# Kernel optimization log

Measured on AMD Instinct MI355X. Metric: run time of the kernel, lower is better.

The kernel has to match this reference:

```python
import jax, jax.numpy as jnp
import numpy as np

IN_F = 4096
OUT_F = 4096
BATCH = 1024

def setup_inputs() -> dict:
    key = jax.random.key(0)
    k = jax.random.split(key, 7)
    x = jax.random.normal(k[0], (BATCH, IN_F), dtype=jnp.float32)
    weight_mu = jax.random.normal(k[1], (OUT_F, IN_F), dtype=jnp.float32) * (1.0 / np.sqrt(IN_F))
    # torch init: uniform(-5,-3) for sigma params (raw values, used directly as std)
    weight_sigma = jax.random.uniform(k[2], (OUT_F, IN_F), dtype=jnp.float32, minval=-5.0, maxval=-3.0)
    bias_mu = jnp.zeros((OUT_F,), dtype=jnp.float32)
    bias_sigma = jax.random.uniform(k[3], (OUT_F,), dtype=jnp.float32, minval=-5.0, maxval=-3.0)
    eps_w = jax.random.normal(k[4], (OUT_F, IN_F), dtype=jnp.float32)
    eps_b = jax.random.normal(k[5], (OUT_F,), dtype=jnp.float32)
    return {"x": x, "weight_mu": weight_mu, "weight_sigma": weight_sigma,
            "bias_mu": bias_mu, "bias_sigma": bias_sigma,
            "eps_w": eps_w, "eps_b": eps_b}

def reference(x, weight_mu, weight_sigma, bias_mu, bias_sigma, eps_w, eps_b):
    # training-mode forward: reparameterized weight sample then dense matmul
    weight = weight_mu + eps_w * weight_sigma        # [out, in]
    bias = bias_mu + eps_b * bias_sigma              # [out]
    # F.linear(x, W, b) = x @ W.T + b
    return jnp.einsum('bi,oi->bo', x, weight) + bias
```

## Files before the change

kernel.cpp:

```cpp
#include <hip/hip_runtime.h>
#include <hip/hip_bf16.h>
#include <stdint.h>

#define M_BATCH 1024
#define N_OUT   4096
#define K_IN    4096

#define BM 128
#define BN 128
#define BK 64
#define KPER  (K_IN / 2)
#define KITER (KPER / BK)

typedef __attribute__((ext_vector_type(8))) __bf16 bf16x8_t;
typedef __attribute__((ext_vector_type(4))) float f32x4_t;
typedef __attribute__((ext_vector_type(4))) float fvec4;

__device__ __forceinline__ unsigned short f2bf_bits(float f) {
    union { __hip_bfloat16 h; unsigned short u; } cvt;
    cvt.h = __float2bfloat16(f);
    return cvt.u;
}

struct __align__(8) US4 { unsigned short x, y, z, w; };

__global__ __launch_bounds__(256) void prep_kernel(
    const float* __restrict__ x,
    const float* __restrict__ wmu,
    const float* __restrict__ wsig,
    const float* __restrict__ epsw,
    unsigned short* __restrict__ wb,
    unsigned short* __restrict__ xb)
{
    const size_t tid = (size_t)blockIdx.x * blockDim.x + threadIdx.x;
    const size_t T   = (size_t)1048576;

    const fvec4* wmu4  = (const fvec4*)wmu;
    const fvec4* wsig4 = (const fvec4*)wsig;
    const fvec4* epsw4 = (const fvec4*)epsw;
    US4* wb4 = (US4*)wb;

    fvec4 m[4], s[4], e[4];
    #pragma unroll
    for (int r = 0; r < 4; ++r) {
        const size_t i = tid + (size_t)r * T;
        m[r] = __builtin_nontemporal_load(wmu4  + i);
        s[r] = __builtin_nontemporal_load(wsig4 + i);
        e[r] = __builtin_nontemporal_load(epsw4 + i);
    }
    #pragma unroll
    for (int r = 0; r < 4; ++r) {
        US4 o;
        o.x = f2bf_bits(fmaf(e[r].x, s[r].x, m[r].x));
        o.y = f2bf_bits(fmaf(e[r].y, s[r].y, m[r].y));
        o.z = f2bf_bits(fmaf(e[r].z, s[r].z, m[r].z));
        o.w = f2bf_bits(fmaf(e[r].w, s[r].w, m[r].w));
        wb4[tid + (size_t)r * T] = o;
    }

    fvec4 v = __builtin_nontemporal_load((const fvec4*)x + tid);
    US4 o;
    o.x = f2bf_bits(v.x);
    o.y = f2bf_bits(v.y);
    o.z = f2bf_bits(v.z);
    o.w = f2bf_bits(v.w);
    ((US4*)xb)[tid] = o;
}

__global__ __launch_bounds__(512, 2) void gemm_bt_kernel(
    const unsigned short* __restrict__ A,
    const unsigned short* __restrict__ B,
    const float* __restrict__ bmu,
    const float* __restrict__ bsig,
    const float* __restrict__ ebias,
    float* __restrict__ C)
{
    __shared__ unsigned short lds[2 * 32768];

    const int t     = threadIdx.x;
    const int bm0   = blockIdx.y * BM;
    const int bn0   = blockIdx.x * BN;
    const int lane  = t & 63;
    const int wave  = t >> 6;
    const int khalf = wave >> 2;
    const int quadw = wave & 3;
    const int wrow  = (quadw >> 1) * 64;
    const int wcol  = (quadw & 1) * 64;
    const int lm    = lane & 15;
    const int quad  = lane >> 4;

    f32x4_t acc[4][4] = {};

    const unsigned short* srcs[8];
    const int rlow = t >> 3;
    const int jsw  = ((t & 7) ^ (rlow & 7)) * 8;
    #pragma unroll
    for (int s = 0; s < 8; ++s) {
        const int row  = rlow + (s & 1) * 64;
        const int half = (s >> 1) & 1;
        const unsigned short* base = (s < 4)
            ? (A + (size_t)(bm0 + row) * K_IN)
            : (B + (size_t)(bn0 + row) * K_IN);
        srcs[s] = base + half * KPER + jsw;
    }
    char* dst0 = (char*)lds + t * 16;

    #pragma unroll
    for (int s = 0; s < 8; ++s)
        __builtin_amdgcn_global_load_lds(
            (const __attribute__((address_space(1))) void*)(srcs[s]),
            (__attribute__((address_space(3))) void*)(dst0 + s * 8192), 16, 0, 0);

    for (int it = 0; it < KITER; ++it) {
        __syncthreads();

        if (it + 1 < KITER) {
            const int koff = (it + 1) * BK;
            const int nb   = ((it + 1) & 1) * 65536;
            #pragma unroll
            for (int s = 0; s < 8; ++s)
                __builtin_amdgcn_global_load_lds(
                    (const __attribute__((address_space(1))) void*)(srcs[s] + koff),
                    (__attribute__((address_space(3))) void*)(dst0 + nb + s * 8192), 16, 0, 0);
        }

        const unsigned short* Lb = lds + (it & 1) * 32768;
        const unsigned short* Ah = Lb + khalf * 8192;
        const unsigned short* Bh = Lb + 16384 + khalf * 8192;

        #pragma unroll
        for (int kk = 0; kk < 2; ++kk) {
            const int p = ((kk * 4) + quad) ^ (lm & 7);
            bf16x8_t a_frag[4], b_frag[4];
            #pragma unroll
            for (int im = 0; im < 4; im++)
                a_frag[im] = *(const bf16x8_t*)(Ah + ((wrow + im * 16 + lm) * 8 + p) * 8);
            #pragma unroll
            for (int jn = 0; jn < 4; jn++)
                b_frag[jn] = *(const bf16x8_t*)(Bh + ((wcol + jn * 16 + lm) * 8 + p) * 8);
            #pragma unroll
            for (int im = 0; im < 4; im++)
                #pragma unroll
                for (int jn = 0; jn < 4; jn++)
                    acc[im][jn] = __builtin_amdgcn_mfma_f32_16x16x32_bf16(
                        a_frag[im], b_frag[jn], acc[im][jn], 0, 0, 0);
        }
    }

    f32x4_t* red = (f32x4_t*)lds;
    if (wave >= 4) {
        #pragma unroll
        for (int im = 0; im < 4; im++)
            #pragma unroll
            for (int jn = 0; jn < 4; jn++)
                red[quadw * 1024 + (im * 4 + jn) * 64 + lane] = acc[im][jn];
    }
    __syncthreads();
    if (wave < 4) {
        #pragma unroll
        for (int jn = 0; jn < 4; jn++) {
            const int gn = bn0 + wcol + jn * 16 + lm;
            const float bias = bmu[gn] + ebias[gn] * bsig[gn];
            #pragma unroll
            for (int im = 0; im < 4; im++) {
                const f32x4_t part = red[quadw * 1024 + (im * 4 + jn) * 64 + lane];
                const int gm0 = bm0 + wrow + im * 16 + quad * 4;
                #pragma unroll
                for (int r = 0; r < 4; r++)
                    C[(size_t)(gm0 + r) * N_OUT + gn] = acc[im][jn][r] + part[r] + bias;
            }
        }
    }
}

__global__ __launch_bounds__(256) void naive_kernel(
    const float* __restrict__ x, const float* __restrict__ wmu,
    const float* __restrict__ wsig, const float* __restrict__ bmu,
    const float* __restrict__ bsig, const float* __restrict__ epsw,
    const float* __restrict__ epsb, float* __restrict__ out)
{
    const int o = blockIdx.x * blockDim.x + threadIdx.x;
    const int b = blockIdx.y;
    const float4* xr = (const float4*)(x + (size_t)b * K_IN);
    const float4* mr = (const float4*)(wmu + (size_t)o * K_IN);
    const float4* sr = (const float4*)(wsig + (size_t)o * K_IN);
    const float4* er = (const float4*)(epsw + (size_t)o * K_IN);
    float s = 0.f;
    for (int k = 0; k < K_IN / 4; k++) {
        float4 xv = xr[k], m = mr[k], sg = sr[k], e = er[k];
        s += xv.x * fmaf(e.x, sg.x, m.x);
        s += xv.y * fmaf(e.y, sg.y, m.y);
        s += xv.z * fmaf(e.z, sg.z, m.z);
        s += xv.w * fmaf(e.w, sg.w, m.w);
    }
    out[(size_t)b * N_OUT + o] = s + bmu[o] + epsb[o] * bsig[o];
}

extern "C" void kernel_launch(void* const* d_in, const int* in_sizes, int n_in,
                              void* d_out, int out_size, void* d_ws, size_t ws_size,
                              hipStream_t stream)
{
    const float* x    = (const float*)d_in[0];
    const float* wmu  = (const float*)d_in[1];
    const float* wsig = (const float*)d_in[2];
    const float* bmu  = (const float*)d_in[3];
    const float* bsig = (const float*)d_in[4];
    const float* epsw = (const float*)d_in[5];
    const float* epsb = (const float*)d_in[6];
    float* out = (float*)d_out;

    const size_t need = ((size_t)N_OUT * K_IN + (size_t)M_BATCH * K_IN) * sizeof(unsigned short);
    if (ws_size >= need) {
        unsigned short* wb = (unsigned short*)d_ws;
        unsigned short* xb = wb + (size_t)N_OUT * K_IN;
        prep_kernel<<<4096, 256, 0, stream>>>(x, wmu, wsig, epsw, wb, xb);
        dim3 grid(N_OUT / BN, M_BATCH / BM);
        gemm_bt_kernel<<<grid, 512, 0, stream>>>(xb, wb, bmu, bsig, epsb, out);
    } else {
        dim3 grid(N_OUT / 256, M_BATCH);
        naive_kernel<<<grid, 256, 0, stream>>>(x, wmu, wsig, bmu, bsig, epsw, epsb, out);
    }
}
```

Before: 242.7 us.

## Fuse prep and GEMM into one cooperative kernel with grid sync

Result: slower. 301.4 us (+24.2%).

```diff
diff --git a/kernel.cpp b/kernel.cpp
--- a/kernel.cpp
+++ b/kernel.cpp
@@ -1,6 +1,9 @@
 #include <hip/hip_runtime.h>
 #include <hip/hip_bf16.h>
+#include <hip/hip_cooperative_groups.h>
 #include <stdint.h>
+
+namespace cg = cooperative_groups;
 
 #define M_BATCH 1024
 #define N_OUT   4096
@@ -22,64 +25,84 @@
     return cvt.u;
 }
 
-struct __align__(8) US4 { unsigned short x, y, z, w; };
-
-__global__ __launch_bounds__(256) void prep_kernel(
+struct __align__(16) US8 { unsigned short s[8]; };
+
+__global__ __launch_bounds__(512, 2) void fused_kernel(
     const float* __restrict__ x,
     const float* __restrict__ wmu,
     const float* __restrict__ wsig,
-    const float* __restrict__ epsw,
-    unsigned short* __restrict__ wb,
-    unsigned short* __restrict__ xb)
-{
-    const size_t tid = (size_t)blockIdx.x * blockDim.x + threadIdx.x;
-    const size_t T   = (size_t)1048576;
-
-    const fvec4* wmu4  = (const fvec4*)wmu;
-    const fvec4* wsig4 = (const fvec4*)wsig;
-    const fvec4* epsw4 = (const fvec4*)epsw;
-    US4* wb4 = (US4*)wb;
-
-    fvec4 m[4], s[4], e[4];
-    #pragma unroll
-    for (int r = 0; r < 4; ++r) {
-        const size_t i = tid + (size_t)r * T;
-        m[r] = __builtin_nontemporal_load(wmu4  + i);
-        s[r] = __builtin_nontemporal_load(wsig4 + i);
-        e[r] = __builtin_nontemporal_load(epsw4 + i);
-    }
-    #pragma unroll
-    for (int r = 0; r < 4; ++r) {
-        US4 o;
-        o.x = f2bf_bits(fmaf(e[r].x, s[r].x, m[r].x));
-        o.y = f2bf_bits(fmaf(e[r].y, s[r].y, m[r].y));
-        o.z = f2bf_bits(fmaf(e[r].z, s[r].z, m[r].z));
-        o.w = f2bf_bits(fmaf(e[r].w, s[r].w, m[r].w));
-        wb4[tid + (size_t)r * T] = o;
-    }
-
-    fvec4 v = __builtin_nontemporal_load((const fvec4*)x + tid);
-    US4 o;
-    o.x = f2bf_bits(v.x);
-    o.y = f2bf_bits(v.y);
-    o.z = f2bf_bits(v.z);
-    o.w = f2bf_bits(v.w);
-    ((US4*)xb)[tid] = o;
-}
-
-__global__ __launch_bounds__(512, 2) void gemm_bt_kernel(
-    const unsigned short* __restrict__ A,
-    const unsigned short* __restrict__ B,
     const float* __restrict__ bmu,
     const float* __restrict__ bsig,
-    const float* __restrict__ ebias,
+    const float* __restrict__ epsw,
+    const float* __restrict__ epsb,
+    unsigned short* __restrict__ wb,
+    unsigned short* __restrict__ xb,
     float* __restrict__ C)
 {
     __shared__ unsigned short lds[2 * 32768];
 
-    const int t     = threadIdx.x;
-    const int bm0   = blockIdx.y * BM;
-    const int bn0   = blockIdx.x * BN;
+    const int t  = threadIdx.x;
+    const int bx = blockIdx.x;
+    const int bn = bx & 31;
+    const int bm = bx >> 5;
+
+    {
+        const size_t base4 = (size_t)bn * 131072 + (size_t)bm * 16384;
+        const size_t base8 = (size_t)bn * 65536  + (size_t)bm * 8192;
+        const fvec4* mu4 = (const fvec4*)wmu;
+        const fvec4* sg4 = (const fvec4*)wsig;
+        const fvec4* ep4 = (const fvec4*)epsw;
+        US8* wb8 = (US8*)wb;
+        #pragma unroll
+        for (int c = 0; c < 16; ++c) {
+            const int u = c * 512 + t;
+            const size_t i4 = base4 + (size_t)u * 2;
+            fvec4 m0 = __builtin_nontemporal_load(mu4 + i4);
+            fvec4 m1 = __builtin_nontemporal_load(mu4 + i4 + 1);
+            fvec4 s0 = __builtin_nontemporal_load(sg4 + i4);
+            fvec4 s1 = __builtin_nontemporal_load(sg4 + i4 + 1);
+            fvec4 e0 = __builtin_nontemporal_load(ep4 + i4);
+            fvec4 e1 = __builtin_nontemporal_load(ep4 + i4 + 1);
+            US8 o;
+            o.s[0] = f2bf_bits(fmaf(e0.x, s0.x, m0.x));
+            o.s[1] = f2bf_bits(fmaf(e0.y, s0.y, m0.y));
+            o.s[2] = f2bf_bits(fmaf(e0.z, s0.z, m0.z));
+            o.s[3] = f2bf_bits(fmaf(e0.w, s0.w, m0.w));
+            o.s[4] = f2bf_bits(fmaf(e1.x, s1.x, m1.x));
+            o.s[5] = f2bf_bits(fmaf(e1.y, s1.y, m1.y));
+            o.s[6] = f2bf_bits(fmaf(e1.z, s1.z, m1.z));
+            o.s[7] = f2bf_bits(fmaf(e1.w, s1.w, m1.w));
+            wb8[base8 + u] = o;
+        }
+
+        const size_t xbase8 = (size_t)bm * 65536 + (size_t)bn * 2048;
+        const fvec4* x4 = (const fvec4*)x;
+        US8* xb8 = (US8*)xb;
+        #pragma unroll
+        for (int c = 0; c < 4; ++c) {
+            const int u = c * 512 + t;
+            const size_t i4 = (xbase8 + u) * 2;
+            fvec4 v0 = __builtin_nontemporal_load(x4 + i4);
+            fvec4 v1 = __builtin_nontemporal_load(x4 + i4 + 1);
+            US8 o;
+            o.s[0] = f2bf_bits(v0.x);
+            o.s[1] = f2bf_bits(v0.y);
+            o.s[2] = f2bf_bits(v0.z);
+            o.s[3] = f2bf_bits(v0.w);
+            o.s[4] = f2bf_bits(v1.x);
+            o.s[5] = f2bf_bits(v1.y);
+            o.s[6] = f2bf_bits(v1.z);
+            o.s[7] = f2bf_bits(v1.w);
+            xb8[xbase8 + u] = o;
+        }
+    }
+
+    cg::this_grid().sync();
+
+    const unsigned short* A = xb;
+    const unsigned short* B = wb;
+    const int bm0   = bm * BM;
+    const int bn0   = bn * BN;
     const int lane  = t & 63;
     const int wave  = t >> 6;
     const int khalf = wave >> 2;
@@ -160,7 +183,7 @@
         #pragma unroll
         for (int jn = 0; jn < 4; jn++) {
             const int gn = bn0 + wcol + jn * 16 + lm;
-            const float bias = bmu[gn] + ebias[gn] * bsig[gn];
+            const float bias = bmu[gn] + epsb[gn] * bsig[gn];
             #pragma unroll
             for (int im = 0; im < 4; im++) {
                 const f32x4_t part = red[quadw * 1024 + (im * 4 + jn) * 64 + lane];
@@ -213,9 +236,11 @@
     if (ws_size >= need) {
         unsigned short* wb = (unsigned short*)d_ws;
         unsigned short* xb = wb + (size_t)N_OUT * K_IN;
-        prep_kernel<<<4096, 256, 0, stream>>>(x, wmu, wsig, epsw, wb, xb);
-        dim3 grid(N_OUT / BN, M_BATCH / BM);
-        gemm_bt_kernel<<<grid, 512, 0, stream>>>(xb, wb, bmu, bsig, epsb, out);
+        void* args[] = { (void*)&x, (void*)&wmu, (void*)&wsig, (void*)&bmu,
+                         (void*)&bsig, (void*)&epsw, (void*)&epsb,
+                         (void*)&wb, (void*)&xb, (void*)&out };
+        hipLaunchCooperativeKernel((const void*)fused_kernel,
+                                   dim3(256), dim3(512), args, 0, stream);
     } else {
         dim3 grid(N_OUT / 256, M_BATCH);
         naive_kernel<<<grid, 256, 0, stream>>>(x, wmu, wsig, bmu, bsig, epsw, epsb, out);
```
